# Kernel optimization log

Hardware: AMD Instinct MI355X
Metric: run time of the kernel (lower is better)

Reference implementation:

```python
import jax, jax.numpy as jnp
import numpy as np

DT = 0.2
N_VAR = 6
FEAT = 32


def _constants():
    dt = DT
    H = np.zeros((2, N_VAR), np.float32); H[0, 0] = 1.0; H[1, 3] = 1.0
    F = np.eye(N_VAR, dtype=np.float32)
    F[0, 1] = dt; F[0, 2] = dt * dt / 2; F[1, 2] = dt
    F[3, 4] = dt; F[3, 5] = dt * dt / 2; F[4, 5] = dt
    G = np.zeros((N_VAR, 2), np.float32)
    G[0, 0] = dt ** 3 / 6; G[1, 0] = dt * dt / 2; G[2, 0] = dt
    G[3, 1] = dt ** 3 / 6; G[4, 1] = dt * dt / 2; G[5, 1] = dt
    Bm = G.copy()  # B matrix equals G_ numerically
    return jnp.asarray(H), jnp.asarray(F), jnp.asarray(G), jnp.asarray(Bm)


def _inv2x2(S):
    a = S[..., 0, 0]; b = S[..., 0, 1]; c = S[..., 1, 0]; d = S[..., 1, 1]
    det = a * d - b * c
    inv = jnp.stack([jnp.stack([d, -b], -1), jnp.stack([-c, a], -1)], -2)
    return inv / det[..., None, None]


def _lstm(x, h, c, Wih, Whh, bih, bhh):
    gates = x @ Wih.T + bih + h @ Whh.T + bhh
    i, f, g, o = jnp.split(gates, 4, axis=-1)
    c2 = jax.nn.sigmoid(f) * c + jax.nn.sigmoid(i) * jnp.tanh(g)
    h2 = jax.nn.sigmoid(o) * jnp.tanh(c2)
    return h2, c2


def _forward(hist, position_std_x, position_std_y, velocity_std_x, velocity_std_y,
             acceleration_std_x, acceleration_std_y, jerk_std, coef_G, GR,
             cf_W, cf_b, lstm_Wih, lstm_Whh, lstm_bih, lstm_bhh, co_W, co_b, len_pred):
    H, F, G, Bm = _constants()
    Bsz = hist.shape[1]
    Z = hist[..., None]                          # (T, B, 2, 1)
    tanhG = jnp.tanh(coef_G)                     # (6,1)
    R = GR[:, None] * GR[None, :]                # (2,2)
    Gs_hist = G * tanhG * jerk_std               # (6,2)
    Q_hist = Gs_hist @ Gs_hist.T                 # (6,6)
    Id = jnp.eye(N_VAR, dtype=hist.dtype)

    # Kalman init
    V0 = (Z[1] - Z[0]) / DT                      # (B,2,1)
    X = jnp.einsum('ij,bjk->bik', H.T, Z[0])     # (B,6,1)
    X = X.at[:, 1, 0].set(V0[:, 0, 0]).at[:, 3, 0].set(V0[:, 1, 0])
    diagv = jnp.concatenate([position_std_x ** 2, velocity_std_x ** 2, acceleration_std_x ** 2,
                             position_std_y ** 2, velocity_std_y ** 2, acceleration_std_y ** 2])
    P = jnp.broadcast_to(jnp.diag(diagv), (Bsz, N_VAR, N_VAR)).astype(hist.dtype)
    h = jnp.zeros((Bsz, FEAT), hist.dtype)
    c = jnp.zeros((Bsz, FEAT), hist.dtype)

    def hist_step(carry, Zt):
        X, P, h, c = carry
        # LSTM state update (command output is discarded during history filtering)
        feat = jnp.tanh(X[:, :, 0] @ cf_W.T + cf_b)
        h, c = _lstm(feat, h, c, lstm_Wih, lstm_Whh, lstm_bih, lstm_bhh)
        # predict (no command)
        X = jnp.einsum('ij,bjk->bik', F, X)
        P = jnp.einsum('ij,bjk,lk->bil', F, P, F) + Q_hist
        # innovation
        y = Zt - jnp.einsum('ij,bjk->bik', H, X)
        S = jnp.einsum('ij,bjk,lk->bil', H, P, H) + R
        # update
        Sinv = _inv2x2(S)
        K = jnp.einsum('bij,kj,bkl->bil', P, H, Sinv)          # (B,6,2)
        X = X + K @ y
        ImKH = Id - jnp.einsum('bij,jk->bik', K, H)
        P = jnp.einsum('bij,bjk,blk->bil', ImKH, P, ImKH) + jnp.einsum('bij,jk,blk->bil', K, R, K)
        return (X, P, h, c), None

    (X, P, h, c), _ = jax.lax.scan(hist_step, (X, P, h, c), Z[1:])

    GtG = G * tanhG                                            # (6,2)

    def pred_step(carry, _):
        X, P, h, c = carry
        feat = jnp.tanh(X[:, :, 0] @ cf_W.T + cf_b)
        h, c = _lstm(feat, h, c, lstm_Wih, lstm_Whh, lstm_bih, lstm_bhh)
        command = h @ co_W.T + co_b                            # (B,4)
        X = jnp.einsum('ij,bjk->bik', F, X) + jnp.einsum('ij,bj->bi', Bm, command[:, :2])[:, :, None]
        Gs = jnp.einsum('ij,bj->bi', GtG, command[:, 2:])      # (B,6)
        Q = jnp.einsum('bi,bj->bij', Gs, Gs)
        P = jnp.einsum('ij,bjk,lk->bil', F, P, F) + Q
        mu = jnp.einsum('ij,bjk->bik', H, X)[:, :, 0]          # (B,2)
        Pout = jnp.einsum('ij,bjk,lk->bil', H, P, H)           # (B,2,2)
        return (X, P, h, c), (mu, Pout)

    _, (mu, Pout) = jax.lax.scan(pred_step, (X, P, h, c), None, length=len_pred)
    sx = jnp.sqrt(Pout[:, :, 0, 0])[..., None]
    sy = jnp.sqrt(Pout[:, :, 1, 1])[..., None]
    rho = (Pout[:, :, 0, 1] + Pout[:, :, 1, 0])[..., None] / (2 * sx * sy)
    return jnp.concatenate([mu, sx, sy, rho], axis=2)          # (len_pred, B, 5)


def setup_inputs() -> dict:
    key = jax.random.key(0)
    ks = jax.random.split(key, 8)
    T, B = 16, 32768
    u = lambda k, shape, fan: jax.random.uniform(k, shape, jnp.float32, -1.0, 1.0) / np.sqrt(fan)
    return {
        'hist': jax.random.normal(ks[0], (T, B, 2), jnp.float32),
        'position_std_x': jnp.ones((1,), jnp.float32) * 0.0519,
        'position_std_y': jnp.ones((1,), jnp.float32) * 1.7321,
        'velocity_std_x': jnp.ones((1,), jnp.float32) * 0.036,
        'velocity_std_y': jnp.ones((1,), jnp.float32) * 19.8837,
        'acceleration_std_x': jnp.ones((1,), jnp.float32) * 1e-05,
        'acceleration_std_y': jnp.ones((1,), jnp.float32) * 5.34,
        'jerk_std': jnp.array([[3.5043, 17.0283]], jnp.float32),
        'coef_G': jnp.array([[0.7427], [2.3545], [-0.0247], [-0.1391], [9.011], [0.0963]], jnp.float32),
        'GR': jnp.array([-0.0015, 0.001], jnp.float32),
        'cf_W': u(ks[1], (FEAT, N_VAR), N_VAR),
        'cf_b': u(ks[2], (FEAT,), N_VAR),
        'lstm_Wih': u(ks[3], (4 * FEAT, FEAT), FEAT),
        'lstm_Whh': u(ks[4], (4 * FEAT, FEAT), FEAT),
        'lstm_bih': u(ks[5], (4 * FEAT,), FEAT),
        'lstm_bhh': u(ks[6], (4 * FEAT,), FEAT),
        'co_W': u(ks[7], (4, FEAT), FEAT),
        'co_b': jnp.zeros((4,), jnp.float32),
        'len_pred': 25,
    }


def reference(hist, position_std_x, position_std_y, velocity_std_x, velocity_std_y,
              acceleration_std_x, acceleration_std_y, jerk_std, coef_G, GR,
              cf_W, cf_b, lstm_Wih, lstm_Whh, lstm_bih, lstm_bhh, co_W, co_b, len_pred):
    return _forward(hist, position_std_x, position_std_y, velocity_std_x, velocity_std_y,
                    acceleration_std_x, acceleration_std_y, jerk_std, coef_G, GR,
                    cf_W, cf_b, lstm_Wih, lstm_Whh, lstm_bih, lstm_bhh, co_W, co_b, int(len_pred))
```

## Files before the change

kernel.cpp:

```cpp
#include <hip/hip_runtime.h>
#include <hip/hip_bf16.h>
#include <math.h>

#define BLK 64
#define EPB 16
#define NF 32
#define THIST 15

typedef __attribute__((ext_vector_type(8))) short s16x8;
typedef __attribute__((ext_vector_type(4))) float f32x4;
typedef __attribute__((ext_vector_type(2))) float f32x2;

union frag_u { s16x8 v; unsigned u[4]; };

#define SWAP3216(A, B) \
    asm("v_permlane32_swap_b32 %0, %1\n\tv_permlane16_swap_b32 %0, %1" \
        : "+v"(A), "+v"(B))

__device__ __forceinline__ float frcp(float x) {
    return __builtin_amdgcn_rcpf(x);
}
__device__ __forceinline__ unsigned packbf2(float x0, float x1) {
    __hip_bfloat162 b = __float22bfloat162_rn(float2{x0, x1});
    union { __hip_bfloat162 b; unsigned u; } c; c.b = b; return c.u;
}
__device__ __forceinline__ float tanhfe(float x) {
    float e = __expf(2.0f * x);
    return fmaf(-2.0f, frcp(e + 1.0f), 1.0f);
}

__device__ __forceinline__ void fpft(float (&P)[6][6]) {
    const float dt = 0.2f, hd = 0.02f;
    #pragma unroll
    for (int j = 0; j < 6; ++j) {
        float a0 = P[0][j] + dt * P[1][j] + hd * P[2][j];
        float a1 = P[1][j] + dt * P[2][j];
        float a3 = P[3][j] + dt * P[4][j] + hd * P[5][j];
        float a4 = P[4][j] + dt * P[5][j];
        P[0][j] = a0; P[1][j] = a1; P[3][j] = a3; P[4][j] = a4;
    }
    #pragma unroll
    for (int i = 0; i < 6; ++i) {
        float a0 = P[i][0] + dt * P[i][1] + hd * P[i][2];
        float a1 = P[i][1] + dt * P[i][2];
        float a3 = P[i][3] + dt * P[i][4] + hd * P[i][5];
        float a4 = P[i][4] + dt * P[i][5];
        P[i][0] = a0; P[i][1] = a1; P[i][3] = a3; P[i][4] = a4;
    }
}

__global__ __launch_bounds__(BLK, 2)
void kalman_lstm(const float* __restrict__ hist,
                 const float* __restrict__ psx, const float* __restrict__ psy,
                 const float* __restrict__ vsx, const float* __restrict__ vsy,
                 const float* __restrict__ asx, const float* __restrict__ asy,
                 const float* __restrict__ jerk, const float* __restrict__ coefG,
                 const float* __restrict__ GRv,
                 const float* __restrict__ cfW, const float* __restrict__ cfb,
                 const float* __restrict__ Wih, const float* __restrict__ Whh,
                 const float* __restrict__ bih, const float* __restrict__ bhh,
                 const float* __restrict__ coW, const float* __restrict__ cob,
                 float* __restrict__ out, int B, int len_pred)
{
    __shared__ float kf[216];

    const int lane = threadIdx.x;
    const int e = lane & 15;
    const int s = lane >> 4;
    const int b = blockIdx.x * EPB + e;

    const float dt = 0.2f, hd = 0.02f;
    const float g0 = dt * dt * dt / 6.0f, g1 = 0.02f, g2 = dt;
    float ga0 = g0 * tanhf(coefG[0]);
    float ga1 = g1 * tanhf(coefG[1]);
    float ga2 = g2 * tanhf(coefG[2]);
    float gb3 = g0 * tanhf(coefG[3]);
    float gb4 = g1 * tanhf(coefG[4]);
    float gb5 = g2 * tanhf(coefG[5]);

    {
        float j0 = jerk[0], j1 = jerk[1];
        float gr0 = GRv[0], gr1 = GRv[1];
        float R00 = gr0 * gr0, R01 = gr0 * gr1, R11 = gr1 * gr1;
        float qa[3] = {ga0 * j0, ga1 * j0, ga2 * j0};
        float qb[3] = {gb3 * j1, gb4 * j1, gb5 * j1};

        float Pk[6][6];
        #pragma unroll
        for (int i = 0; i < 6; ++i)
            #pragma unroll
            for (int j = 0; j < 6; ++j) Pk[i][j] = 0.0f;
        { float v;
          v = psx[0]; Pk[0][0] = v * v;
          v = vsx[0]; Pk[1][1] = v * v;
          v = asx[0]; Pk[2][2] = v * v;
          v = psy[0]; Pk[3][3] = v * v;
          v = vsy[0]; Pk[4][4] = v * v;
          v = asy[0]; Pk[5][5] = v * v; }

        #pragma unroll 1
        for (int t = 0; t < THIST; ++t) {
            fpft(Pk);
            #pragma unroll
            for (int i = 0; i < 3; ++i)
                #pragma unroll
                for (int j = 0; j < 3; ++j) {
                    Pk[i][j]         += qa[i] * qa[j];
                    Pk[3 + i][3 + j] += qb[i] * qb[j];
                }
            float S00 = Pk[0][0] + R00;
            float S01 = Pk[0][3] + R01;
            float S11 = Pk[3][3] + R11;
            float idet = 1.0f / (S00 * S11 - S01 * S01);
            float i00 =  S11 * idet, i01 = -S01 * idet, i11 = S00 * idet;
            float K0[6], K1[6];
            #pragma unroll
            for (int i = 0; i < 6; ++i) {
                K0[i] = Pk[i][0] * i00 + Pk[i][3] * i01;
                K1[i] = Pk[i][0] * i01 + Pk[i][3] * i11;
            }
            if (lane == 0) {
                #pragma unroll
                for (int i = 0; i < 3; ++i) {
                    kf[t * 12 + 2 * i]     = K0[i];
                    kf[t * 12 + 2 * i + 1] = K0[3 + i];
                    kf[t * 12 + 6 + 2 * i]     = K1[i];
                    kf[t * 12 + 6 + 2 * i + 1] = K1[3 + i];
                }
            }
            #pragma unroll
            for (int i = 0; i < 6; ++i) {
                Pk[i][1] -= K0[1] * Pk[i][0] + K1[1] * Pk[i][3];
                Pk[i][2] -= K0[2] * Pk[i][0] + K1[2] * Pk[i][3];
                Pk[i][4] -= K0[4] * Pk[i][0] + K1[4] * Pk[i][3];
                Pk[i][5] -= K0[5] * Pk[i][0] + K1[5] * Pk[i][3];
                float t0 = Pk[i][0] - (K0[0] * Pk[i][0] + K1[0] * Pk[i][3]);
                float t3 = Pk[i][3] - (K0[3] * Pk[i][0] + K1[3] * Pk[i][3]);
                Pk[i][0] = t0; Pk[i][3] = t3;
            }
        }
        if (lane == 0) {
            #pragma unroll
            for (int i = 0; i < 6; ++i)
                #pragma unroll
                for (int j = 0; j < 6; ++j) kf[180 + i * 6 + j] = Pk[i][j];
        }
    }

    s16x8 wih_h[8], whh_h[8];
    #pragma unroll
    for (int nt = 0; nt < 8; ++nt) {
        int base = (nt * 16 + e) * NF + s * 8;
        frag_u ih_h, hh_h;
        #pragma unroll
        for (int q = 0; q < 4; ++q) {
            ih_h.u[q] = packbf2(Wih[base + 2 * q], Wih[base + 2 * q + 1]);
            hh_h.u[q] = packbf2(Whh[base + 2 * q], Whh[base + 2 * q + 1]);
        }
        wih_h[nt] = ih_h.v;
        whh_h[nt] = hh_h.v;
    }

    f32x4 biasF[8];
    #pragma unroll
    for (int nt = 0; nt < 8; ++nt) {
        int base = nt * 16 + 4 * s;
        f32x4 bi = *(const f32x4*)&bih[base];
        f32x4 bh = *(const f32x4*)&bhh[base];
        biasF[nt] = bi + bh;
    }

    s16x8 cfwA0, cfwA1;
    {
        frag_u fa0, fa1; fa0.v = (s16x8)0; fa1.v = (s16x8)0;
        if (s == 0) {
            const float* w0 = cfW + e * 6;
            const float* w1 = cfW + (16 + e) * 6;
            fa0.u[0] = packbf2(w0[0], w0[1]);
            fa0.u[1] = packbf2(w0[2], w0[3]);
            fa0.u[2] = packbf2(w0[4], w0[5]);
            fa0.u[3] = packbf2(cfb[e], 0.0f);
            fa1.u[0] = packbf2(w1[0], w1[1]);
            fa1.u[1] = packbf2(w1[2], w1[3]);
            fa1.u[2] = packbf2(w1[4], w1[5]);
            fa1.u[3] = packbf2(cfb[16 + e], 0.0f);
        }
        cfwA0 = fa0.v; cfwA1 = fa1.v;
    }
    s16x8 cmdA;
    {
        frag_u ca;
        const float* cp = coW + (e & 3) * NF + 8 * s;
        #pragma unroll
        for (int q = 0; q < 4; ++q)
            ca.u[q] = packbf2(cp[2 * q], cp[2 * q + 1]);
        cmdA = ca.v;
    }
    f32x4 cobC = {cob[0], cob[1], cob[2], cob[3]};

    const float2* hist2 = (const float2*)hist;
    float2 z0 = hist2[b];
    float2 z1 = hist2[B + b];
    f32x2 Xa = {z0.x, (z1.y - z0.y) / dt};
    f32x2 Xb = {(z1.x - z0.x) / dt, 0.0f};
    f32x2 Xc = {0.0f, 0.0f};

    float creg[8];
    #pragma unroll
    for (int j = 0; j < 8; ++j) creg[j] = 0.0f;
    s16x8 ah_h = (s16x8)0;

    __syncthreads();

    auto lstm_step = [&]() {
        frag_u xb;
        xb.u[0] = packbf2(Xa.x, Xb.x);
        xb.u[1] = packbf2(Xc.x, Xa.y);
        xb.u[2] = packbf2(Xb.y, Xc.y);
        xb.u[3] = 0x00003f80u;
        const f32x4 zc4 = {0.0f, 0.0f, 0.0f, 0.0f};
        f32x4 fp0 = __builtin_amdgcn_mfma_f32_16x16x32_bf16(cfwA0, xb.v, zc4, 0, 0, 0);
        f32x4 fp1 = __builtin_amdgcn_mfma_f32_16x16x32_bf16(cfwA1, xb.v, zc4, 0, 0, 0);
        auto tanhq = [](float x) {
            float eg = __expf(2.0f * x);
            return fmaf(-2.0f, frcp(eg + 1.0f), 1.0f);
        };
        unsigned F00 = packbf2(tanhq(fp0[0]), tanhq(fp0[1]));
        unsigned F01 = packbf2(tanhq(fp0[2]), tanhq(fp0[3]));
        unsigned F10 = packbf2(tanhq(fp1[0]), tanhq(fp1[1]));
        unsigned F11 = packbf2(tanhq(fp1[2]), tanhq(fp1[3]));
        frag_u af;
        { unsigned A = F00, Bv = F10; SWAP3216(A, Bv); af.u[0] = A; af.u[2] = Bv; }
        { unsigned A = F01, Bv = F11; SWAP3216(A, Bv); af.u[1] = A; af.u[3] = Bv; }

        f32x4 acc[8];
        #pragma unroll
        for (int nt = 0; nt < 8; ++nt) {
            acc[nt] = __builtin_amdgcn_mfma_f32_16x16x32_bf16(wih_h[nt], af.v, biasF[nt], 0, 0, 0);
            acc[nt] = __builtin_amdgcn_mfma_f32_16x16x32_bf16(whh_h[nt], ah_h, acc[nt], 0, 0, 0);
        }

        unsigned whx[2][2];
        #pragma unroll
        for (int blk = 0; blk < 2; ++blk) {
            float hv[4];
            #pragma unroll
            for (int r = 0; r < 4; ++r) {
                float gi = acc[0 + blk][r];
                float gf = acc[2 + blk][r];
                float gg = acc[4 + blk][r];
                float go = acc[6 + blk][r];
                float ef = __expf(-gf);
                float ei = __expf(-gi);
                float eg = __expf(2.0f * gg);
                float r1 = frcp(1.0f + ef);
                float r2 = frcp((1.0f + ei) * (eg + 1.0f));
                float cn = fmaf(eg - 1.0f, r2, creg[4 * blk + r] * r1);
                creg[4 * blk + r] = cn;
                float eo = __expf(-go);
                float ec = __expf(2.0f * cn);
                hv[r] = (ec - 1.0f) * frcp((1.0f + eo) * (ec + 1.0f));
            }
            #pragma unroll
            for (int rp = 0; rp < 2; ++rp)
                whx[blk][rp] = packbf2(hv[2 * rp], hv[2 * rp + 1]);
        }

        frag_u ahh;
        { unsigned A = whx[0][0], Bv = whx[1][0]; SWAP3216(A, Bv); ahh.u[0] = A; ahh.u[2] = Bv; }
        { unsigned A = whx[0][1], Bv = whx[1][1]; SWAP3216(A, Bv); ahh.u[1] = A; ahh.u[3] = Bv; }
        ah_h = ahh.v;
    };

    float2 zc = z1;
    #pragma unroll 1
    for (int t = 0; t < THIST; ++t) {
        int tn = (t + 2 < 16) ? (t + 2) : 15;
        float2 zn = hist2[(size_t)tn * B + b];
        f32x4 k0 = *(const f32x4*)&kf[t * 12];
        f32x4 k1 = *(const f32x4*)&kf[t * 12 + 4];
        f32x4 k2 = *(const f32x4*)&kf[t * 12 + 8];

        lstm_step();

        Xa = Xa + dt * Xb + hd * Xc;
        Xb = Xb + dt * Xc;
        float y0 = zc.x - Xa.x, y1 = zc.y - Xa.y;
        f32x2 kA0 = {k0[0], k0[1]}, kB0 = {k0[2], k0[3]}, kC0 = {k1[0], k1[1]};
        f32x2 kA1 = {k1[2], k1[3]}, kB1 = {k2[0], k2[1]}, kC1 = {k2[2], k2[3]};
        Xa = Xa + kA0 * y0 + kA1 * y1;
        Xb = Xb + kB0 * y0 + kB1 * y1;
        Xc = Xc + kC0 * y0 + kC1 * y1;
        zc = zn;
    }

    f32x2 pxy00 = {kf[180], kf[201]}, pxy01 = {kf[181], kf[202]},
          pxy02 = {kf[182], kf[203]}, pxy11 = {kf[187], kf[208]},
          pxy12 = {kf[188], kf[209]}, pxy22 = {kf[194], kf[214]};
    float c00 = kf[183], c01 = kf[184], c02 = kf[185],
          c10 = kf[189], c11 = kf[190], c12 = kf[191],
          c20 = kf[195], c21 = kf[196], c22 = kf[197];
    const f32x2 gaP0 = {ga0, gb3}, gaP1 = {ga1, gb4}, gaP2 = {ga2, gb5};

    #pragma unroll 1
    for (int tp = 0; tp < len_pred; ++tp) {
        lstm_step();

        f32x4 cm = __builtin_amdgcn_mfma_f32_16x16x32_bf16(cmdA, ah_h, cobC, 0, 0, 0);
        f32x2 cmdP  = {cm[0], cm[1]};
        f32x2 cmd23 = {cm[2], cm[3]};

        Xa = Xa + dt * Xb + hd * Xc + g0 * cmdP;
        Xb = Xb + dt * Xc + g1 * cmdP;
        Xc = Xc + g2 * cmdP;

        f32x2 gsA = gaP0 * cmd23;
        f32x2 gsB = gaP1 * cmd23;
        f32x2 gsC = gaP2 * cmd23;
        {
            f32x2 r00 = pxy00 + dt * pxy01 + hd * pxy02;
            f32x2 r01 = pxy01 + dt * pxy11 + hd * pxy12;
            f32x2 r02 = pxy02 + dt * pxy12 + hd * pxy22;
            f32x2 r11 = pxy11 + dt * pxy12;
            f32x2 r12 = pxy12 + dt * pxy22;
            pxy00 = r00 + dt * r01 + hd * r02;
            pxy01 = r01 + dt * r02;
            pxy02 = r02;
            pxy11 = r11 + dt * r12;
            pxy12 = r12;
            pxy00 += gsA * gsA; pxy01 += gsA * gsB; pxy02 += gsA * gsC;
            pxy11 += gsB * gsB; pxy12 += gsB * gsC; pxy22 += gsC * gsC;
        }
        {
            float gs0 = gsA.x, gs1 = gsB.x, gs2 = gsC.x;
            float gs3 = gsA.y, gs4 = gsB.y, gs5 = gsC.y;
            float q00 = c00 + dt * c10 + hd * c20;
            float q01 = c01 + dt * c11 + hd * c21;
            float q02 = c02 + dt * c12 + hd * c22;
            float q10 = c10 + dt * c20;
            float q11 = c11 + dt * c21;
            float q12 = c12 + dt * c22;
            c00 = q00 + dt * q01 + hd * q02;
            c01 = q01 + dt * q02;
            c02 = q02;
            c10 = q10 + dt * q11 + hd * q12;
            c11 = q11 + dt * q12;
            c12 = q12;
            float n20 = c20 + dt * c21 + hd * c22;
            float n21 = c21 + dt * c22;
            c20 = n20; c21 = n21;
            c00 += gs0 * gs3; c01 += gs0 * gs4; c02 += gs0 * gs5;
            c10 += gs1 * gs3; c11 += gs1 * gs4; c12 += gs1 * gs5;
            c20 += gs2 * gs3; c21 += gs2 * gs4; c22 += gs2 * gs5;
        }

        float sx = sqrtf(pxy00.x), sy = sqrtf(pxy00.y);
        float rho = c00 / (sx * sy);
        if (s == 0) {
            size_t o = ((size_t)tp * B + b) * 5u;
            out[o + 0] = Xa.x;
            out[o + 1] = Xa.y;
            out[o + 2] = sx;
            out[o + 3] = sy;
            out[o + 4] = rho;
        }
    }
}

extern "C" void kernel_launch(void* const* d_in, const int* in_sizes, int n_in,
                              void* d_out, int out_size, void* d_ws, size_t ws_size,
                              hipStream_t stream) {
    const int T = 16;
    const int B = in_sizes[0] / (2 * T);
    const int len_pred = out_size / (5 * B);
    (void)d_ws; (void)ws_size; (void)n_in;

    const int grid = (B + EPB - 1) / EPB;
    kalman_lstm<<<grid, BLK, 0, stream>>>(
        (const float*)d_in[0],  (const float*)d_in[1],  (const float*)d_in[2],
        (const float*)d_in[3],  (const float*)d_in[4],  (const float*)d_in[5],
        (const float*)d_in[6],  (const float*)d_in[7],  (const float*)d_in[8],
        (const float*)d_in[9],  (const float*)d_in[10], (const float*)d_in[11],
        (const float*)d_in[12], (const float*)d_in[13], (const float*)d_in[14],
        (const float*)d_in[15], (const float*)d_in[16], (const float*)d_in[17],
        (float*)d_out, B, len_pred);
}
```

Baseline: 189.5 us.

## Permute LSTM weight rows to drop permlane swaps and fold -log2e into weights

Reorders the LSTM gate-weight rows, bias and input-feature rows so the MFMA output layout already matches the B-operand fragment layout of the next MFMA. This removes the permlane32/16 swap instructions on the recurrent critical path. It also pre-scales the sigmoid gate weights and biases by -log2(e) so the sigmoids can use exp2 directly without a multiply. Folding the scale in before the bf16 conversion shifts rounding slightly.

```diff
diff --git a/kernel.cpp b/kernel.cpp
--- a/kernel.cpp
+++ b/kernel.cpp
@@ -12,10 +12,6 @@
 typedef __attribute__((ext_vector_type(2))) float f32x2;
 
 union frag_u { s16x8 v; unsigned u[4]; };
-
-#define SWAP3216(A, B) \
-    asm("v_permlane32_swap_b32 %0, %1\n\tv_permlane16_swap_b32 %0, %1" \
-        : "+v"(A), "+v"(B))
 
 __device__ __forceinline__ float frcp(float x) {
     return __builtin_amdgcn_rcpf(x);
@@ -71,6 +67,7 @@
 
     const float dt = 0.2f, hd = 0.02f;
     const float g0 = dt * dt * dt / 6.0f, g1 = 0.02f, g2 = dt;
+    const float NL2E = -1.4426950408889634f;
     float ga0 = g0 * tanhf(coefG[0]);
     float ga1 = g1 * tanhf(coefG[1]);
     float ga2 = g2 * tanhf(coefG[2]);
@@ -150,12 +147,14 @@
     s16x8 wih_h[8], whh_h[8];
     #pragma unroll
     for (int nt = 0; nt < 8; ++nt) {
-        int base = (nt * 16 + e) * NF + s * 8;
+        int G = nt >> 1, blk = nt & 1;
+        float sc = (G == 2) ? 1.0f : NL2E;
+        int base = (G * 32 + 8 * (e >> 2) + 4 * blk + (e & 3)) * NF + s * 8;
         frag_u ih_h, hh_h;
         #pragma unroll
         for (int q = 0; q < 4; ++q) {
-            ih_h.u[q] = packbf2(Wih[base + 2 * q], Wih[base + 2 * q + 1]);
-            hh_h.u[q] = packbf2(Whh[base + 2 * q], Whh[base + 2 * q + 1]);
+            ih_h.u[q] = packbf2(sc * Wih[base + 2 * q], sc * Wih[base + 2 * q + 1]);
+            hh_h.u[q] = packbf2(sc * Whh[base + 2 * q], sc * Whh[base + 2 * q + 1]);
         }
         wih_h[nt] = ih_h.v;
         whh_h[nt] = hh_h.v;
@@ -164,26 +163,30 @@
     f32x4 biasF[8];
     #pragma unroll
     for (int nt = 0; nt < 8; ++nt) {
-        int base = nt * 16 + 4 * s;
+        int G = nt >> 1, blk = nt & 1;
+        float sc = (G == 2) ? 1.0f : NL2E;
+        int base = G * 32 + 8 * s + 4 * blk;
         f32x4 bi = *(const f32x4*)&bih[base];
         f32x4 bh = *(const f32x4*)&bhh[base];
-        biasF[nt] = bi + bh;
+        biasF[nt] = (bi + bh) * sc;
     }
 
     s16x8 cfwA0, cfwA1;
     {
         frag_u fa0, fa1; fa0.v = (s16x8)0; fa1.v = (s16x8)0;
         if (s == 0) {
-            const float* w0 = cfW + e * 6;
-            const float* w1 = cfW + (16 + e) * 6;
+            int f0 = 8 * (e >> 2) + (e & 3);
+            int f1 = f0 + 4;
+            const float* w0 = cfW + f0 * 6;
+            const float* w1 = cfW + f1 * 6;
             fa0.u[0] = packbf2(w0[0], w0[1]);
             fa0.u[1] = packbf2(w0[2], w0[3]);
             fa0.u[2] = packbf2(w0[4], w0[5]);
-            fa0.u[3] = packbf2(cfb[e], 0.0f);
+            fa0.u[3] = packbf2(cfb[f0], 0.0f);
             fa1.u[0] = packbf2(w1[0], w1[1]);
             fa1.u[1] = packbf2(w1[2], w1[3]);
             fa1.u[2] = packbf2(w1[4], w1[5]);
-            fa1.u[3] = packbf2(cfb[16 + e], 0.0f);
+            fa1.u[3] = packbf2(cfb[f1], 0.0f);
         }
         cfwA0 = fa0.v; cfwA1 = fa1.v;
     }
@@ -225,13 +228,11 @@
             float eg = __expf(2.0f * x);
             return fmaf(-2.0f, frcp(eg + 1.0f), 1.0f);
         };
-        unsigned F00 = packbf2(tanhq(fp0[0]), tanhq(fp0[1]));
-        unsigned F01 = packbf2(tanhq(fp0[2]), tanhq(fp0[3]));
-        unsigned F10 = packbf2(tanhq(fp1[0]), tanhq(fp1[1]));
-        unsigned F11 = packbf2(tanhq(fp1[2]), tanhq(fp1[3]));
         frag_u af;
-        { unsigned A = F00, Bv = F10; SWAP3216(A, Bv); af.u[0] = A; af.u[2] = Bv; }
-        { unsigned A = F01, Bv = F11; SWAP3216(A, Bv); af.u[1] = A; af.u[3] = Bv; }
+        af.u[0] = packbf2(tanhq(fp0[0]), tanhq(fp0[1]));
+        af.u[1] = packbf2(tanhq(fp0[2]), tanhq(fp0[3]));
+        af.u[2] = packbf2(tanhq(fp1[0]), tanhq(fp1[1]));
+        af.u[3] = packbf2(tanhq(fp1[2]), tanhq(fp1[3]));
 
         f32x4 acc[8];
         #pragma unroll
@@ -246,18 +247,18 @@
             float hv[4];
             #pragma unroll
             for (int r = 0; r < 4; ++r) {
-                float gi = acc[0 + blk][r];
-                float gf = acc[2 + blk][r];
-                float gg = acc[4 + blk][r];
-                float go = acc[6 + blk][r];
-                float ef = __expf(-gf);
-                float ei = __expf(-gi);
+                float gis = acc[0 + blk][r];
+                float gfs = acc[2 + blk][r];
+                float gg  = acc[4 + blk][r];
+                float gos = acc[6 + blk][r];
+                float ef = exp2f(gfs);
+                float ei = exp2f(gis);
                 float eg = __expf(2.0f * gg);
                 float r1 = frcp(1.0f + ef);
                 float r2 = frcp((1.0f + ei) * (eg + 1.0f));
                 float cn = fmaf(eg - 1.0f, r2, creg[4 * blk + r] * r1);
                 creg[4 * blk + r] = cn;
-                float eo = __expf(-go);
+                float eo = exp2f(gos);
                 float ec = __expf(2.0f * cn);
                 hv[r] = (ec - 1.0f) * frcp((1.0f + eo) * (ec + 1.0f));
             }
@@ -267,8 +268,10 @@
         }
 
         frag_u ahh;
-        { unsigned A = whx[0][0], Bv = whx[1][0]; SWAP3216(A, Bv); ahh.u[0] = A; ahh.u[2] = Bv; }
-        { unsigned A = whx[0][1], Bv = whx[1][1]; SWAP3216(A, Bv); ahh.u[1] = A; ahh.u[3] = Bv; }
+        ahh.u[0] = whx[0][0];
+        ahh.u[1] = whx[0][1];
+        ahh.u[2] = whx[1][0];
+        ahh.u[3] = whx[1][1];
         ah_h = ahh.v;
     };
 
```

New measurement: 199.9 us. 1.05x slower.
